# Performance work log

Measured on AMD Instinct MI355X. Metric: run time of the kernel, lower is better.

## Reference

```python
import jax, jax.numpy as jnp
import numpy as np

N_CHANNELS = 3
WIN_SIZES = (5, 11, 17)
C1 = 0.01 ** 2
C2 = 0.03 ** 2


def _gaussian_filter(n_channels, win_size, sigma):
    h = win_size // 2
    r = np.arange(-h, h + 1, dtype=np.float32)
    yy, xx = np.meshgrid(r, r, indexing='ij')
    g = np.exp(-0.5 * ((xx ** 2 + yy ** 2) / (2.0 * sigma ** 2)))
    g = np.tile(g[None, None], (n_channels, 1, 1, 1))  # [C,1,k,k] OIHW depthwise
    g = g / g.sum()
    return jnp.asarray(g, dtype=jnp.float32)


def _dconv(x, f, k):
    # depthwise conv, 'same' zero padding (torch F.conv2d default padding behavior)
    p = k // 2
    return jax.lax.conv_general_dilated(
        x, f, window_strides=(1, 1), padding=[(p, p), (p, p)],
        feature_group_count=x.shape[1],
        dimension_numbers=('NCHW', 'OIHW', 'NCHW'))


def _ssim_score(b1, b2, g, k):
    mu1 = _dconv(b1, g, k)
    mu2 = _dconv(b2, g, k)
    mu1_sq = mu1 * mu1
    mu2_sq = mu2 * mu2
    mu1_mu2 = mu1 * mu2
    sigma1_sq = jnp.abs(_dconv(b1 * b1, g, k) - mu1_sq)
    sigma2_sq = jnp.abs(_dconv(b2 * b2, g, k) - mu2_sq)
    sigma12 = _dconv(b1 * b2, g, k) - mu1_mu2
    ssim = (2 * mu1_mu2 + C1) * (2 * sigma12 + C2) / ((mu1_sq + mu2_sq + C1) * (sigma1_sq + sigma2_sq + C2))
    res = jnp.clip(ssim, -1.0, 1.0)
    res = (res + 1.0) / 2.0
    return 1.0 - res


def setup_inputs() -> dict:
    key = jax.random.key(0)
    k1, k2 = jax.random.split(key)
    B, C, H, W = 32, N_CHANNELS, 512, 512
    inp = {
        'batch1': jax.random.uniform(k1, (B, C, H, W), dtype=jnp.float32),
        'batch2': jax.random.uniform(k2, (B, C, H, W), dtype=jnp.float32),
    }
    for i, w in enumerate(WIN_SIZES):
        inp[f'g_filter_{i}'] = _gaussian_filter(C, w, w / 7.0)
    return inp


def reference(batch1, batch2, g_filter_0, g_filter_1, g_filter_2):
    filters = (g_filter_0, g_filter_1, g_filter_2)
    sim = jnp.zeros_like(batch1)
    for g, k in zip(filters, WIN_SIZES):
        sim = sim + _ssim_score(batch1, batch2, g, k)
    sim = sim / len(WIN_SIZES)
    sim = (sim + 1.0) / 2.0
    return 1.0 - sim
```

## Files before the change

kernel.cpp:

```cpp
#include <hip/hip_runtime.h>

#define IMG_H 512
#define IMG_W 512
#define WOUT  128
#define WV    144
#define SP    296
#define SB    148
#define NRING 24
#define RS    8
#define NSTEP 8
#define SVP   152
#define PS    (RS * SVP)
#define C1F   1.0e-4f
#define C2F   9.0e-4f

__global__ void prep_weights_kernel(const float* __restrict__ g0,
                                    const float* __restrict__ g1,
                                    const float* __restrict__ g2,
                                    float* __restrict__ ws) {
  if (blockIdx.x == 0 && threadIdx.x == 0) {
    const float* gs[3] = {g0, g1, g2};
    const int ks[3]  = {5, 11, 17};
    const int off[3] = {0, 8, 32};
    for (int s = 0; s < 3; ++s) {
      const float* g = gs[s];
      int k = ks[s], h = k / 2;
      double rs = 1.0 / sqrt((double)g[h * k + h]);
      for (int j = 0; j < k; ++j)
        ws[off[s] + j] = (float)((double)g[h * k + j] * rs);
    }
  }
}

__device__ __forceinline__ float to_sgpr(float x) {
  int i = __builtin_amdgcn_readfirstlane(__builtin_bit_cast(int, x));
  return __builtin_bit_cast(float, i);
}

__device__ __forceinline__ int mod24(int x) {
  return x - 24 * ((x * 2731) >> 16);
}

template<int NROWS>
__device__ __forceinline__ void stage_rows(const float* __restrict__ p1,
                                           const float* __restrict__ p2,
                                           float* __restrict__ sin_,
                                           int gr0, int x0, int tid) {
  constexpr int NT = NROWS * 36;
  for (int t = tid; t < NT; t += 256) {
    int rr = (t * 1821) >> 16;
    int c4 = t - rr * 36;
    int gr = gr0 + rr;
    int gc = x0 - 8 + 4 * c4;
    float4 v1 = make_float4(0.f, 0.f, 0.f, 0.f);
    float4 v2 = make_float4(0.f, 0.f, 0.f, 0.f);
    if ((unsigned)gr < (unsigned)IMG_H && (unsigned)gc < (unsigned)IMG_W) {
      int o = gr * IMG_W + gc;
      v1 = *(const float4*)(p1 + o);
      v2 = *(const float4*)(p2 + o);
    }
    int slot = mod24(gr + 56);
    float* p = sin_ + slot * SP + 4 * c4;
    *(float4*)(p)      = v1;
    *(float4*)(p + SB) = v2;
  }
}

template<int K>
__device__ __forceinline__ void v_col2(const float (&wk)[K],
                                       const float* __restrict__ sin_,
                                       float* __restrict__ sv_,
                                       int yc, int t) {
  constexpr int HK = K / 2;
  const int rp = (t * 1821) >> 16;
  const int cc = t - rp * 36;
  const int r0 = rp * 2;
  const int cb = 4 * cc;

  float acc[4][2][4];
  #pragma unroll
  for (int d = 0; d < 4; ++d)
    #pragma unroll
    for (int r = 0; r < 2; ++r)
      #pragma unroll
      for (int j = 0; j < 4; ++j) acc[d][r][j] = 0.f;

  const int us = mod24(yc + r0 + (8 - HK));
  const float* pA = sin_ + us * SP + cb;
  const float* pB = pA - NRING * SP;

  #pragma unroll
  for (int i = 0; i <= K; ++i) {
    const float* row = (us + i < NRING) ? pA : pB;
    float4 A  = *(const float4*)(row + i * SP);
    float4 Bv = *(const float4*)(row + i * SP + SB);
    float x[4] = {A.x, A.y, A.z, A.w};
    float y[4] = {Bv.x, Bv.y, Bv.z, Bv.w};
    float pp[4], qq[4];
    #pragma unroll
    for (int j = 0; j < 4; ++j) {
      pp[j] = fmaf(x[j], x[j], y[j] * y[j]);
      qq[j] = x[j] * y[j];
    }
    if (i < K) {
      const float w = wk[i];
      #pragma unroll
      for (int j = 0; j < 4; ++j) {
        acc[0][0][j] = fmaf(w, x[j],  acc[0][0][j]);
        acc[1][0][j] = fmaf(w, y[j],  acc[1][0][j]);
        acc[2][0][j] = fmaf(w, pp[j], acc[2][0][j]);
        acc[3][0][j] = fmaf(w, qq[j], acc[3][0][j]);
      }
    }
    if (i > 0) {
      const float w = wk[i - 1];
      #pragma unroll
      for (int j = 0; j < 4; ++j) {
        acc[0][1][j] = fmaf(w, x[j],  acc[0][1][j]);
        acc[1][1][j] = fmaf(w, y[j],  acc[1][1][j]);
        acc[2][1][j] = fmaf(w, pp[j], acc[2][1][j]);
        acc[3][1][j] = fmaf(w, qq[j], acc[3][1][j]);
      }
    }
  }

  #pragma unroll
  for (int d = 0; d < 4; ++d) {
    #pragma unroll
    for (int r = 0; r < 2; ++r) {
      float* vb = sv_ + d * PS + (r0 + r) * SVP + cb;
      *(float4*)vb = make_float4(acc[d][r][0], acc[d][r][1],
                                 acc[d][r][2], acc[d][r][3]);
    }
  }
}

template<int K>
__device__ __forceinline__ void h_col(const float (&wk)[K],
                                      const float* __restrict__ sv_,
                                      int rr, int g, float (&accs)[4]) {
  constexpr int OFF = 8 - K / 2;
  float conv[4][4];
  #pragma unroll
  for (int d = 0; d < 4; ++d) {
    const float* vb = sv_ + d * PS + rr * SVP + 4 * g;
    float win[20];
    if constexpr (K == 5) {
      #pragma unroll
      for (int q = 1; q < 4; ++q) {
        float4 t4 = *(const float4*)(vb + 4 * q);
        win[4*q+0] = t4.x; win[4*q+1] = t4.y; win[4*q+2] = t4.z; win[4*q+3] = t4.w;
      }
    } else {
      #pragma unroll
      for (int q = 0; q < 5; ++q) {
        float4 t4 = *(const float4*)(vb + 4 * q);
        win[4*q+0] = t4.x; win[4*q+1] = t4.y; win[4*q+2] = t4.z; win[4*q+3] = t4.w;
      }
    }
    #pragma unroll
    for (int j = 0; j < 4; ++j) {
      float s = 0.f;
      #pragma unroll
      for (int t = 0; t < K; ++t) s = fmaf(wk[t], win[j + t + OFF], s);
      conv[d][j] = s;
    }
  }
  #pragma unroll
  for (int j = 0; j < 4; ++j) {
    float mu1 = conv[0][j], mu2 = conv[1][j];
    float P = conv[2][j], Q = conv[3][j];
    float mu11 = mu1 * mu1, mu22 = mu2 * mu2, mu12 = mu1 * mu2;
    float sg12 = Q - mu12;
    float sgS  = P - mu11 - mu22;
    float num  = fmaf(2.f, mu12, C1F) * fmaf(2.f, sg12, C2F);
    float den  = (mu11 + mu22 + C1F) * (sgS + C2F);
    float ssim = __fdividef(num, den);
    accs[j] += fminf(1.f, fmaxf(-1.f, ssim));
  }
}

__global__ __launch_bounds__(256, 3)
void mssim_kernel(const float* __restrict__ b1, const float* __restrict__ b2,
                  const float* __restrict__ ws, float* __restrict__ out) {
  __shared__ __attribute__((aligned(16))) float sin_[NRING * SP];
  __shared__ __attribute__((aligned(16))) float sv_[4 * PS];

  const int tid = threadIdx.x;
  const int bid = blockIdx.x;
  const int img = bid >> 5;
  const int rem = bid & 31;
  const int y0  = (rem >> 2) * (RS * NSTEP);
  const int x0  = (rem & 3) * WOUT;
  const float* p1 = b1 + img * (IMG_H * IMG_W);
  const float* p2 = b2 + img * (IMG_H * IMG_W);
  float*       po = out + img * (IMG_H * IMG_W);

  float w17[17], w11[11], w5[5];
  #pragma unroll
  for (int i = 0; i < 17; ++i) w17[i] = to_sgpr(ws[32 + i]);
  #pragma unroll
  for (int i = 0; i < 11; ++i) w11[i] = to_sgpr(ws[8 + i]);
  #pragma unroll
  for (int i = 0; i < 5;  ++i) w5[i]  = to_sgpr(ws[i]);

  stage_rows<16>(p1, p2, sin_, y0 - 8, x0, tid);

  const int hr = tid >> 5;
  const int hg = tid & 31;
  const bool vact = tid < 144;

  #pragma unroll 1
  for (int step = 0; step < NSTEP; ++step) {
    const int yc = y0 + step * RS;
    stage_rows<RS>(p1, p2, sin_, yc + 8, x0, tid);
    __syncthreads();

    float accs[4] = {0.f, 0.f, 0.f, 0.f};

    if (vact) v_col2<17>(w17, sin_, sv_, yc, tid);
    __syncthreads();
    h_col<17>(w17, sv_, hr, hg, accs);
    __syncthreads();

    if (vact) v_col2<11>(w11, sin_, sv_, yc, tid);
    __syncthreads();
    h_col<11>(w11, sv_, hr, hg, accs);
    __syncthreads();

    if (vact) v_col2<5>(w5, sin_, sv_, yc, tid);
    __syncthreads();
    h_col<5>(w5, sv_, hr, hg, accs);

    float4 o = make_float4(0.25f + accs[0] * (1.f / 12.f),
                           0.25f + accs[1] * (1.f / 12.f),
                           0.25f + accs[2] * (1.f / 12.f),
                           0.25f + accs[3] * (1.f / 12.f));
    *(float4*)(po + (yc + hr) * IMG_W + x0 + 4 * hg) = o;
  }
}

extern "C" void kernel_launch(void* const* d_in, const int* in_sizes, int n_in,
                              void* d_out, int out_size, void* d_ws, size_t ws_size,
                              hipStream_t stream) {
  const float* b1 = (const float*)d_in[0];
  const float* b2 = (const float*)d_in[1];
  const float* g0 = (const float*)d_in[2];
  const float* g1 = (const float*)d_in[3];
  const float* g2 = (const float*)d_in[4];
  float* ws  = (float*)d_ws;
  float* out = (float*)d_out;

  prep_weights_kernel<<<1, 64, 0, stream>>>(g0, g1, g2, ws);
  mssim_kernel<<<3072, 256, 0, stream>>>(b1, b2, ws, out);
}
```

Measured before the change: 536.9 us.

## Prefetch next step's input rows with idle warps during vertical passes

The shared ring buffer grows from 24 to 28 rows. The separate per-step staging phase is removed. The otherwise idle threads 192-255 now load the next step's 8 rows in three chunks, one during each vertical convolution pass, writing only into slots that no remaining pass still reads. This is meant to hide global-load latency behind compute instead of stalling all threads on staging at the start of each step. In exchange, shared memory use rises, the initial prologue loads more rows, and the slot-reuse timing across the three window sizes becomes more delicate.

New measurement: 517.0 us. 1.04x faster.

```diff
diff --git a/kernel.cpp b/kernel.cpp
--- a/kernel.cpp
+++ b/kernel.cpp
@@ -6,7 +6,7 @@
 #define WV    144
 #define SP    296
 #define SB    148
-#define NRING 24
+#define NRING 28
 #define RS    8
 #define NSTEP 8
 #define SVP   152
@@ -37,9 +37,10 @@
   return __builtin_bit_cast(float, i);
 }
 
-__device__ __forceinline__ int mod24(int x) {
-  return x - 24 * ((x * 2731) >> 16);
-}
+__device__ __forceinline__ int mod28(int x) {
+  return x - 28 * ((x * 9363) >> 18);
+}
+
 
 template<int NROWS>
 __device__ __forceinline__ void stage_rows(const float* __restrict__ p1,
@@ -59,7 +60,32 @@
       v1 = *(const float4*)(p1 + o);
       v2 = *(const float4*)(p2 + o);
     }
-    int slot = mod24(gr + 56);
+    int slot = mod28(gr + 12 + 28);
+    float* p = sin_ + slot * SP + 4 * c4;
+    *(float4*)(p)      = v1;
+    *(float4*)(p + SB) = v2;
+  }
+}
+
+template<int NR>
+__device__ __forceinline__ void stage_span(const float* __restrict__ p1,
+                                           const float* __restrict__ p2,
+                                           float* __restrict__ sin_,
+                                           int gr0, int x0, int st) {
+  constexpr int NT = NR * 36;
+  for (int t = st; t < NT; t += 64) {
+    int rr = (t * 1821) >> 16;
+    int c4 = t - rr * 36;
+    int gr = gr0 + rr;
+    int gc = x0 - 8 + 4 * c4;
+    float4 v1 = make_float4(0.f, 0.f, 0.f, 0.f);
+    float4 v2 = make_float4(0.f, 0.f, 0.f, 0.f);
+    if ((unsigned)gr < (unsigned)IMG_H && (unsigned)gc < (unsigned)IMG_W) {
+      int o = gr * IMG_W + gc;
+      v1 = *(const float4*)(p1 + o);
+      v2 = *(const float4*)(p2 + o);
+    }
+    int slot = mod28(gr + 12);
     float* p = sin_ + slot * SP + 4 * c4;
     *(float4*)(p)      = v1;
     *(float4*)(p + SB) = v2;
@@ -85,7 +111,7 @@
       #pragma unroll
       for (int j = 0; j < 4; ++j) acc[d][r][j] = 0.f;
 
-  const int us = mod24(yc + r0 + (8 - HK));
+  const int us = mod28(yc + r0 + (12 - HK));
   const float* pA = sin_ + us * SP + cb;
   const float* pB = pA - NRING * SP;
 
@@ -204,31 +230,35 @@
   #pragma unroll
   for (int i = 0; i < 5;  ++i) w5[i]  = to_sgpr(ws[i]);
 
-  stage_rows<16>(p1, p2, sin_, y0 - 8, x0, tid);
+  stage_rows<24>(p1, p2, sin_, y0 - 8, x0, tid);
 
   const int hr = tid >> 5;
   const int hg = tid & 31;
   const bool vact = tid < 144;
+  const int  st   = tid - 192;
 
   #pragma unroll 1
   for (int step = 0; step < NSTEP; ++step) {
     const int yc = y0 + step * RS;
-    stage_rows<RS>(p1, p2, sin_, yc + 8, x0, tid);
+    const bool do_stage = (st >= 0) && (step < NSTEP - 1);
     __syncthreads();
 
     float accs[4] = {0.f, 0.f, 0.f, 0.f};
 
     if (vact) v_col2<17>(w17, sin_, sv_, yc, tid);
+    else if (do_stage) stage_span<4>(p1, p2, sin_, yc + 16, x0, st);
     __syncthreads();
     h_col<17>(w17, sv_, hr, hg, accs);
     __syncthreads();
 
     if (vact) v_col2<11>(w11, sin_, sv_, yc, tid);
+    else if (do_stage) stage_span<3>(p1, p2, sin_, yc + 20, x0, st);
     __syncthreads();
     h_col<11>(w11, sv_, hr, hg, accs);
     __syncthreads();
 
     if (vact) v_col2<5>(w5, sin_, sv_, yc, tid);
+    else if (do_stage) stage_span<1>(p1, p2, sin_, yc + 23, x0, st);
     __syncthreads();
     h_col<5>(w5, sv_, hr, hg, accs);
 
```
